# Optimization experiments

Hardware: AMD Instinct MI355X
Metric: run time of the kernel (lower is better)

## Reference

```python
import jax, jax.numpy as jnp
import numpy as np

EPS = 1e-7  # Keras backend epsilon


def setup_inputs() -> dict:
    key = jax.random.key(0)
    kx, ka, ke, kp = jax.random.split(key, 4)
    B, N, F, K_, C = 8, 2048, 128, 128, 128
    X = jax.random.normal(kx, (B, N, F), dtype=jnp.float32)
    Au = (jax.random.uniform(ka, (B, N, N)) < 0.05).astype(jnp.float32)
    A = jnp.maximum(Au, jnp.swapaxes(Au, -1, -2))
    W_emb = jax.random.normal(ke, (F, C), dtype=jnp.float32) * 0.1
    W_pool = jax.random.normal(kp, (F, K_), dtype=jnp.float32) * 0.1
    return {"X": X, "A": A, "W_emb": W_emb, "W_pool": W_pool}


def _diffpool(X, A, W_emb, W_pool):
    N = A.shape[-1]
    I = jnp.eye(N, dtype=A.dtype)
    A_ = A + I
    # symmetric normalization D^-1/2 (A+I) D^-1/2
    d = jax.lax.rsqrt(jnp.sum(A_, axis=-1))          # [B, N]
    fltr = A_ * d[..., :, None] * d[..., None, :]    # [B, N, N]

    Z = jnp.einsum('bnm,bmc->bnc', fltr, X @ W_emb)  # embedding GNN (no activation)
    S = jax.nn.softmax(jnp.einsum('bnm,bmk->bnk', fltr, X @ W_pool), axis=-1)  # [B, N, k]

    # link prediction loss: ||A - S S^T||_F per graph, mean over batch
    S_gram = jnp.einsum('bnk,bmk->bnm', S, S)
    LP_loss = jnp.mean(jnp.linalg.norm(A - S_gram, ord='fro', axis=(-1, -2)))

    # entropy loss on assignments
    entr = -jnp.sum(S * jnp.log(S + EPS), axis=-1)   # [B, N]
    entr_loss = jnp.mean(entr)

    X_pooled = jnp.einsum('bnk,bnc->bkc', S, Z)                  # S^T Z
    A_pooled = jnp.einsum('bnk,bnm,bml->bkl', S, A, S)           # S^T A S
    return X_pooled, A_pooled, S, LP_loss, entr_loss


def reference(X, A, W_emb, W_pool):
    return _diffpool(X, A, W_emb, W_pool)
```

## Files before the change

### kernel.cpp

```cpp
#include <hip/hip_runtime.h>
#include <math.h>

typedef __bf16 bf16x8 __attribute__((ext_vector_type(8)));
typedef float  f32x4  __attribute__((ext_vector_type(4)));
typedef unsigned short u16x4 __attribute__((ext_vector_type(4)));

#define DEVI __device__ __forceinline__

static constexpr int NB  = 8;
static constexpr int NN  = 2048;
static constexpr int NF  = 128;
static constexpr int NC2 = 256;

static constexpr int OUT_X0  = 0;
static constexpr int OUT_A0  = NB * 128 * 128;
static constexpr int OUT_S0  = OUT_A0 + NB * 128 * 128;
static constexpr int OUT_LP  = OUT_S0 + NB * NN * 128;
static constexpr int OUT_ENT = OUT_LP + 1;

DEVI unsigned short f2b(float f) {
  unsigned int u = __builtin_bit_cast(unsigned int, f);
  u += 0x7fffu + ((u >> 16) & 1u);
  return (unsigned short)(u >> 16);
}
DEVI float b2f(unsigned short h) {
  unsigned int u = ((unsigned int)h) << 16;
  return __builtin_bit_cast(float, u);
}
DEVI void load_lds16(const void* g, void* l) {
  __builtin_amdgcn_global_load_lds(
      (const __attribute__((address_space(1))) void*)g,
      (__attribute__((address_space(3))) void*)l, 16, 0, 0);
}

DEVI void stage_tile(const unsigned short* src, int ld, unsigned short* dst,
                     int k0, int tid) {
  const int wave = tid >> 6;
#pragma unroll
  for (int is = 0; is < 2; ++is) {
    const int row = is * 64 + (tid >> 2);
    const int c   = tid & 3;
    const unsigned short* g = src + row * ld + k0 + ((c ^ (row & 3)) << 3);
    unsigned short* l = dst + ((is * 256 + wave * 64) << 3);
    load_lds16(g, l);
  }
}

DEVI void gemm_core(const unsigned short* Aop, int lda,
                    const unsigned short* Bop, int ldb, int ksteps,
                    unsigned short* lA0, unsigned short* lA1,
                    unsigned short* lB0, unsigned short* lB1,
                    int tid, f32x4 (&acc)[4][4]) {
  const int lane = tid & 63;
  const int wave = tid >> 6;
  const int wr = wave >> 1, wc = wave & 1;
  const int l15 = lane & 15;
  const int sx = (lane >> 4) ^ (l15 & 3);
#pragma unroll
  for (int i = 0; i < 4; ++i) {
#pragma unroll
    for (int j = 0; j < 4; ++j) acc[i][j] = (f32x4){0.f, 0.f, 0.f, 0.f};
  }
  stage_tile(Aop, lda, lA0, 0, tid);
  stage_tile(Bop, ldb, lB0, 0, tid);
  __syncthreads();
  for (int kt = 0; kt < ksteps; ++kt) {
    unsigned short* curA = (kt & 1) ? lA1 : lA0;
    unsigned short* curB = (kt & 1) ? lB1 : lB0;
    if (kt + 1 < ksteps) {
      unsigned short* nxtA = (kt & 1) ? lA0 : lA1;
      unsigned short* nxtB = (kt & 1) ? lB0 : lB1;
      stage_tile(Aop, lda, nxtA, (kt + 1) * 32, tid);
      stage_tile(Bop, ldb, nxtB, (kt + 1) * 32, tid);
    }
    bf16x8 af[4], bg[4];
#pragma unroll
    for (int i = 0; i < 4; ++i) {
      const int row = wr * 64 + i * 16 + l15;
      af[i] = *(const bf16x8*)(curA + ((row * 4 + sx) << 3));
    }
#pragma unroll
    for (int j = 0; j < 4; ++j) {
      const int col = wc * 64 + j * 16 + l15;
      bg[j] = *(const bf16x8*)(curB + ((col * 4 + sx) << 3));
    }
#pragma unroll
    for (int i = 0; i < 4; ++i) {
#pragma unroll
      for (int j = 0; j < 4; ++j)
        acc[i][j] = __builtin_amdgcn_mfma_f32_16x16x32_bf16(af[i], bg[j],
                                                            acc[i][j], 0, 0, 0);
    }
    __syncthreads();
  }
}


__global__ __launch_bounds__(256) void k_prep_a(const float* __restrict__ A,
                                                unsigned short* __restrict__ AB,
                                                float* __restrict__ dvec,
                                                float* __restrict__ rsum) {
  const int row = blockIdx.x * 4 + (threadIdx.x >> 6);
  const int lane = threadIdx.x & 63;
  const f32x4* src = (const f32x4*)(A + ((size_t)row << 11));
  u16x4* dst = (u16x4*)(AB + ((size_t)row << 11));
  float s = 0.f;
#pragma unroll
  for (int it = 0; it < 8; ++it) {
    f32x4 v = src[it * 64 + lane];
    s += v[0] + v[1] + v[2] + v[3];
    u16x4 o;
    o[0] = f2b(v[0]); o[1] = f2b(v[1]); o[2] = f2b(v[2]); o[3] = f2b(v[3]);
    dst[it * 64 + lane] = o;
  }
#pragma unroll
  for (int o2 = 32; o2; o2 >>= 1) s += __shfl_down(s, o2);
  if (lane == 0) {
    dvec[row] = rsqrtf(s + 1.f);
    rsum[row] = s;
  }
}

__global__ __launch_bounds__(256) void k_conv_xw(const float* __restrict__ X,
                                                 const float* __restrict__ Wemb,
                                                 const float* __restrict__ Wpool,
                                                 unsigned short* __restrict__ XB,
                                                 unsigned short* __restrict__ WT) {
  const int blk = blockIdx.x, tid = threadIdx.x;
  if (blk < 512) {
    const int i0 = blk * 1024 + tid;
    const f32x4* src = (const f32x4*)X;
    u16x4* dst = (u16x4*)XB;
#pragma unroll
    for (int it = 0; it < 4; ++it) {
      const int idx = i0 + it * 256;
      f32x4 v = src[idx];
      u16x4 o;
      o[0] = f2b(v[0]); o[1] = f2b(v[1]); o[2] = f2b(v[2]); o[3] = f2b(v[3]);
      dst[idx] = o;
    }
  } else {
    const int e = (blk - 512) * 256 + tid;
    const int c = e >> 4, f0 = (e & 15) * 8;
    const float* W = (c < 128) ? Wemb : Wpool;
    const int cc = c & 127;
#pragma unroll
    for (int q = 0; q < 8; ++q)
      WT[c * 128 + f0 + q] = f2b(W[(f0 + q) * 128 + cc]);
  }
}

__global__ __launch_bounds__(256) void k_gemm_xw(const unsigned short* __restrict__ XB,
                                                 const unsigned short* __restrict__ WT,
                                                 const float* __restrict__ dvec,
                                                 unsigned short* __restrict__ VT) {
  __shared__ unsigned short lA[2][4096], lB[2][4096];
  const int mt = blockIdx.x, ct = blockIdx.y, tid = threadIdx.x;
  f32x4 acc[4][4];
  gemm_core(XB + mt * 128 * NF, NF, WT + ct * 128 * NF, NF, NF / 32,
            lA[0], lA[1], lB[0], lB[1], tid, acc);
  const int lane = tid & 63, wave = tid >> 6;
  const int wr = wave >> 1, wc = wave & 1, l15 = lane & 15, l4 = (lane >> 4) * 4;
#pragma unroll
  for (int i = 0; i < 4; ++i) {
    const int gr0 = mt * 128 + wr * 64 + i * 16 + l4;
    const int b = gr0 >> 11, n0 = gr0 & 2047;
    const f32x4 dv = *(const f32x4*)(dvec + gr0);
#pragma unroll
    for (int j = 0; j < 4; ++j) {
      const int gc = ct * 128 + wc * 64 + j * 16 + l15;
      u16x4 pk;
#pragma unroll
      for (int r = 0; r < 4; ++r) pk[r] = f2b(acc[i][j][r] * dv[r]);
      *(u16x4*)(VT + (((size_t)(b * NC2 + gc)) << 11) + n0) = pk;
    }
  }
}

__global__ __launch_bounds__(256) void k_gemm_nv(const unsigned short* __restrict__ AB,
                                                 const unsigned short* __restrict__ VT,
                                                 const float* __restrict__ dvec,
                                                 unsigned short* __restrict__ YT,
                                                 float* __restrict__ out,
                                                 float* __restrict__ entv) {
  __shared__ unsigned short lA[2][4096], lB[2][4096];
  const int mt = blockIdx.x, ct = blockIdx.y, b = blockIdx.z, tid = threadIdx.x;
  const unsigned short* Aop = AB + ((size_t)b << 22) + (size_t)mt * 128 * NN;
  const unsigned short* Bop = VT + (((size_t)(b * NC2 + ct * 128)) << 11);
  f32x4 acc[4][4];
  gemm_core(Aop, NN, Bop, NN, NN / 32, lA[0], lA[1], lB[0], lB[1], tid, acc);
  const int lane = tid & 63, wave = tid >> 6;
  const int wr = wave >> 1, wc = wave & 1, l15 = lane & 15, l4g = lane >> 4;
  const int l4 = l4g * 4;
  f32x4 dv[4];
#pragma unroll
  for (int i = 0; i < 4; ++i) {
    const int n0 = mt * 128 + wr * 64 + i * 16 + l4;
    dv[i] = *(const f32x4*)(dvec + (b << 11) + n0);
  }
#pragma unroll
  for (int i = 0; i < 4; ++i) {
    const int n0 = mt * 128 + wr * 64 + i * 16 + l4;
#pragma unroll
    for (int j = 0; j < 4; ++j) {
      const int c = ct * 128 + wc * 64 + j * 16 + l15;
      const u16x4 vv = *(const u16x4*)(VT + (((size_t)(b * NC2 + c)) << 11) + n0);
#pragma unroll
      for (int r = 0; r < 4; ++r)
        acc[i][j][r] = (acc[i][j][r] + b2f(vv[r])) * dv[i][r];
    }
  }
  if (ct == 0) {
#pragma unroll
    for (int i = 0; i < 4; ++i) {
      const int n0 = mt * 128 + wr * 64 + i * 16 + l4;
#pragma unroll
      for (int j = 0; j < 4; ++j) {
        const int c = wc * 64 + j * 16 + l15;
        u16x4 pk;
#pragma unroll
        for (int r = 0; r < 4; ++r) pk[r] = f2b(acc[i][j][r]);
        *(u16x4*)(YT + (((size_t)(b * 384 + c)) << 11) + n0) = pk;
      }
    }
    return;
  }
  float* mbuf = (float*)lA;
  float* sbuf = mbuf + 256;
  float* tbuf = mbuf + 512;
  float* ebuf = mbuf + 768;
  float rm[4][4], rs[4][4], rt[4][4];
#pragma unroll
  for (int i = 0; i < 4; ++i)
#pragma unroll
    for (int r = 0; r < 4; ++r) {
      float m = fmaxf(fmaxf(acc[i][0][r], acc[i][1][r]),
                      fmaxf(acc[i][2][r], acc[i][3][r]));
#pragma unroll
      for (int off = 1; off < 16; off <<= 1) m = fmaxf(m, __shfl_xor(m, off));
      if (l15 == 0) mbuf[(wr * 2 + wc) * 64 + i * 16 + l4 + r] = m;
    }
  __syncthreads();
#pragma unroll
  for (int i = 0; i < 4; ++i)
#pragma unroll
    for (int r = 0; r < 4; ++r) {
      const int row = i * 16 + l4 + r;
      rm[i][r] = fmaxf(mbuf[(wr * 2) * 64 + row], mbuf[(wr * 2 + 1) * 64 + row]);
      rs[i][r] = 0.f; rt[i][r] = 0.f;
    }
#pragma unroll
  for (int i = 0; i < 4; ++i)
#pragma unroll
    for (int j = 0; j < 4; ++j)
#pragma unroll
      for (int r = 0; r < 4; ++r) {
        const float xm = acc[i][j][r] - rm[i][r];
        const float e = __expf(xm);
        acc[i][j][r] = e;
        rs[i][r] += e;
        rt[i][r] += xm * e;
      }
  __syncthreads();
#pragma unroll
  for (int i = 0; i < 4; ++i)
#pragma unroll
    for (int r = 0; r < 4; ++r) {
      float s = rs[i][r], t = rt[i][r];
#pragma unroll
      for (int off = 1; off < 16; off <<= 1) {
        s += __shfl_xor(s, off); t += __shfl_xor(t, off);
      }
      if (l15 == 0) {
        sbuf[(wr * 2 + wc) * 64 + i * 16 + l4 + r] = s;
        tbuf[(wr * 2 + wc) * 64 + i * 16 + l4 + r] = t;
      }
    }
  __syncthreads();
  float ent = 0.f;
#pragma unroll
  for (int i = 0; i < 4; ++i)
#pragma unroll
    for (int r = 0; r < 4; ++r) {
      const int row = i * 16 + l4 + r;
      const float s = sbuf[(wr * 2) * 64 + row] + sbuf[(wr * 2 + 1) * 64 + row];
      const float t = tbuf[(wr * 2) * 64 + row] + tbuf[(wr * 2 + 1) * 64 + row];
      const float inv = 1.f / s;
      rs[i][r] = inv;
      ent += __logf(s) - t * inv;
    }
#pragma unroll
  for (int i = 0; i < 4; ++i) {
    const int n0 = mt * 128 + wr * 64 + i * 16 + l4;
#pragma unroll
    for (int j = 0; j < 4; ++j) {
      const int c = wc * 64 + j * 16 + l15;
      u16x4 pk;
#pragma unroll
      for (int r = 0; r < 4; ++r) {
        const float sv = acc[i][j][r] * rs[i][r];
        pk[r] = f2b(sv);
        out[OUT_S0 + (((size_t)((b << 11) + n0 + r)) << 7) + c] = sv;
      }
      *(u16x4*)(YT + (((size_t)(b * 384 + 256 + c)) << 11) + n0) = pk;
    }
  }
  if (wc == 0 && l15 == 0) ebuf[wr * 4 + l4g] = ent;
  __syncthreads();
  if (tid == 0) {
    float e8 = 0.f;
#pragma unroll
    for (int q = 0; q < 8; ++q) e8 += ebuf[q];
    entv[b * 16 + mt] = e8;
  }
}

__global__ __launch_bounds__(256) void k_gemm_as(const unsigned short* __restrict__ AB,
                                                 unsigned short* __restrict__ YT) {
  __shared__ unsigned short lA[2][2048], lB[2][4096];
  const int mt = blockIdx.x, b = blockIdx.z, tid = threadIdx.x;
  const unsigned short* Aop = AB + ((size_t)b << 22) + (size_t)mt * 64 * NN;
  const unsigned short* Bop = YT + (((size_t)(b * 384 + 256)) << 11);
  const int lane = tid & 63, wave = tid >> 6;
  const int l15 = lane & 15;
  const int sx = (lane >> 4) ^ (l15 & 3);
  f32x4 acc[4][2];
#pragma unroll
  for (int i = 0; i < 4; ++i) {
    acc[i][0] = (f32x4){0.f, 0.f, 0.f, 0.f};
    acc[i][1] = (f32x4){0.f, 0.f, 0.f, 0.f};
  }
  {
    const int row = tid >> 2, c = tid & 3;
    load_lds16(Aop + row * NN + ((c ^ (row & 3)) << 3), lA[0] + (wave << 9));
  }
  stage_tile(Bop, NN, lB[0], 0, tid);
  __syncthreads();
  for (int kt = 0; kt < 64; ++kt) {
    unsigned short* curA = lA[kt & 1];
    unsigned short* curB = lB[kt & 1];
    if (kt + 1 < 64) {
      const int k0 = (kt + 1) * 32;
      const int row = tid >> 2, c = tid & 3;
      load_lds16(Aop + row * NN + k0 + ((c ^ (row & 3)) << 3),
                 lA[(kt + 1) & 1] + (wave << 9));
      stage_tile(Bop, NN, lB[(kt + 1) & 1], k0, tid);
    }
    bf16x8 af[4], bg[2];
#pragma unroll
    for (int i = 0; i < 4; ++i)
      af[i] = *(const bf16x8*)(curA + (((i * 16 + l15) * 4 + sx) << 3));
#pragma unroll
    for (int j = 0; j < 2; ++j) {
      const int col = wave * 32 + j * 16 + l15;
      bg[j] = *(const bf16x8*)(curB + ((col * 4 + sx) << 3));
    }
#pragma unroll
    for (int i = 0; i < 4; ++i) {
#pragma unroll
      for (int j = 0; j < 2; ++j)
        acc[i][j] = __builtin_amdgcn_mfma_f32_16x16x32_bf16(af[i], bg[j],
                                                            acc[i][j], 0, 0, 0);
    }
    __syncthreads();
  }
  const int l4 = (lane >> 4) * 4;
#pragma unroll
  for (int i = 0; i < 4; ++i) {
    const int n0 = mt * 64 + i * 16 + l4;
#pragma unroll
    for (int j = 0; j < 2; ++j) {
      const int c = wave * 32 + j * 16 + l15;
      u16x4 pk;
#pragma unroll
      for (int r = 0; r < 4; ++r) pk[r] = f2b(acc[i][j][r]);
      *(u16x4*)(YT + (((size_t)(b * 384 + 128 + c)) << 11) + n0) = pk;
    }
  }
}

__global__ __launch_bounds__(256) void k_gemm_p(const unsigned short* __restrict__ YT,
                                                float* __restrict__ Pp) {
  __shared__ unsigned short lA[2][4096], lB[2][4096];
  const int ct = blockIdx.x, sk = blockIdx.y, b = blockIdx.z, tid = threadIdx.x;
  const unsigned short* Aop = YT + (((size_t)(b * 384 + 256)) << 11) + sk * 256;
  const unsigned short* Bop = YT + (((size_t)(b * 384 + ct * 128)) << 11) + sk * 256;
  f32x4 acc[4][4];
  gemm_core(Aop, NN, Bop, NN, 8, lA[0], lA[1], lB[0], lB[1], tid, acc);
  const int lane = tid & 63, wave = tid >> 6;
  const int wr = wave >> 1, wc = wave & 1, l15 = lane & 15, l4 = (lane >> 4) * 4;
  float* dst = Pp + ((size_t)(sk * NB + b)) * 128 * 384;
#pragma unroll
  for (int i = 0; i < 4; ++i) {
    const int p0 = wr * 64 + i * 16 + l4;
#pragma unroll
    for (int j = 0; j < 4; ++j) {
      const int gc = ct * 128 + wc * 64 + j * 16 + l15;
#pragma unroll
      for (int r = 0; r < 4; ++r) dst[(p0 + r) * 384 + gc] = acc[i][j][r];
    }
  }
}

__global__ __launch_bounds__(256) void k_reduce_p(const float* __restrict__ Pp,
                                                  float* __restrict__ trp,
                                                  float* __restrict__ g2p,
                                                  float* __restrict__ out) {
  const int chunk = blockIdx.x, b = blockIdx.y, tid = threadIdx.x;
  const int e = chunk * 256 + tid;
  const int p = e / 384, c = e - p * 384;
  float s = 0.f;
#pragma unroll
  for (int sk = 0; sk < 8; ++sk)
    s += Pp[((size_t)(sk * NB + b)) * (128 * 384) + e];
  float tr = 0.f, g2 = 0.f;
  if (c < 128) {
    out[OUT_X0 + ((size_t)(b * 128 + p)) * 128 + c] = s;
  } else if (c < 256) {
    out[OUT_A0 + ((size_t)(b * 128 + p)) * 128 + (c - 128)] = s;
    if (c - 128 == p) tr = s;
  } else {
    g2 = s * s;
  }
  __shared__ float rb[512];
  rb[tid] = tr; rb[256 + tid] = g2;
  __syncthreads();
  for (int o = 128; o; o >>= 1) {
    if (tid < o) { rb[tid] += rb[tid + o]; rb[256 + tid] += rb[256 + tid + o]; }
    __syncthreads();
  }
  if (tid == 0) { trp[b * 192 + chunk] = rb[0]; g2p[b * 192 + chunk] = rb[256]; }
}

__global__ __launch_bounds__(256) void k_lp(const float* __restrict__ rsum,
                                            const float* __restrict__ trp,
                                            const float* __restrict__ g2p,
                                            float* __restrict__ lpv) {
  const int b = blockIdx.x, tid = threadIdx.x;
  float nz = 0.f;
#pragma unroll
  for (int i = 0; i < 8; ++i) nz += rsum[(b << 11) + i * 256 + tid];
  float tr = (tid < 192) ? trp[b * 192 + tid] : 0.f;
  float g2 = (tid < 192) ? g2p[b * 192 + tid] : 0.f;
  __shared__ float rb[768];
  rb[tid] = nz; rb[256 + tid] = tr; rb[512 + tid] = g2;
  __syncthreads();
  for (int o = 128; o; o >>= 1) {
    if (tid < o) {
      rb[tid] += rb[tid + o];
      rb[256 + tid] += rb[256 + tid + o];
      rb[512 + tid] += rb[512 + tid + o];
    }
    __syncthreads();
  }
  if (tid == 0)
    lpv[b] = sqrtf(fmaxf(rb[0] - 2.f * rb[256] + rb[512], 0.f));
}

__global__ __launch_bounds__(256) void k_losses(const float* __restrict__ entv,
                                                const float* __restrict__ lpv,
                                                float* __restrict__ out) {
  const int tid = threadIdx.x;
  __shared__ float rb[256];
  rb[tid] = (tid < 128) ? entv[tid] : 0.f;
  __syncthreads();
  for (int o = 128; o; o >>= 1) {
    if (tid < o) rb[tid] += rb[tid + o];
    __syncthreads();
  }
  if (tid == 0) {
    float lp = 0.f;
#pragma unroll
    for (int b = 0; b < 8; ++b) lp += lpv[b];
    out[OUT_LP] = 0.125f * lp;
    out[OUT_ENT] = rb[0] * (1.f / (NB * NN));
  }
}

extern "C" void kernel_launch(void* const* d_in, const int* in_sizes, int n_in,
                              void* d_out, int out_size, void* d_ws, size_t ws_size,
                              hipStream_t stream) {
  const float* X     = (const float*)d_in[0];
  const float* A     = (const float*)d_in[1];
  const float* Wemb  = (const float*)d_in[2];
  const float* Wpool = (const float*)d_in[3];
  float* out = (float*)d_out;

  char* ws = (char*)d_ws;
  size_t o = 0;
  unsigned short* AB = (unsigned short*)(ws + o); o += (size_t)NB * NN * NN * 2;
  unsigned short* XB = (unsigned short*)(ws + o); o += (size_t)NB * NN * NF * 2;
  unsigned short* WT = (unsigned short*)(ws + o); o += (size_t)NC2 * NF * 2;
  unsigned short* VT = (unsigned short*)(ws + o); o += (size_t)NB * NC2 * NN * 2;
  unsigned short* YT = (unsigned short*)(ws + o); o += (size_t)NB * 384 * NN * 2;
  float* Pp  = (float*)(ws + o); o += (size_t)8 * NB * 128 * 384 * 4;
  float* dvec = (float*)(ws + o); o += (size_t)NB * NN * 4;
  float* rsum = (float*)(ws + o); o += (size_t)NB * NN * 4;
  float* trp  = (float*)(ws + o); o += (size_t)NB * 192 * 4;
  float* g2p  = (float*)(ws + o); o += (size_t)NB * 192 * 4;
  float* entv = (float*)(ws + o); o += 128 * 4;
  float* lpv  = (float*)(ws + o); o += NB * 4;

  k_prep_a  <<<dim3(NB * NN / 4), 256, 0, stream>>>(A, AB, dvec, rsum);
  k_conv_xw <<<dim3(528), 256, 0, stream>>>(X, Wemb, Wpool, XB, WT);
  k_gemm_xw <<<dim3(NB * NN / 128, 2), 256, 0, stream>>>(XB, WT, dvec, VT);
  k_gemm_nv <<<dim3(NN / 128, 2, NB), 256, 0, stream>>>(AB, VT, dvec, YT, out, entv);
  k_gemm_as <<<dim3(NN / 64, 1, NB), 256, 0, stream>>>(AB, YT);
  k_gemm_p  <<<dim3(3, 8, NB), 256, 0, stream>>>(YT, Pp);
  k_reduce_p<<<dim3(192, NB), 256, 0, stream>>>(Pp, trp, g2p, out);
  k_lp      <<<dim3(NB), 256, 0, stream>>>(rsum, trp, g2p, lpv);
  k_losses  <<<1, 256, 0, stream>>>(entv, lpv, out);
}
```

Baseline: 323.5 us.

## Shrink GEMM M-tiles to 64 rows, double split-K, fuse prep kernels, change LDS swizzle

The two prep kernels are merged into one launch. The NxN-by-V and X-by-W GEMMs move from 128x128 to 64x128 tiles, which doubles the block count and improves CU occupancy, since the original grid had only 256 blocks. The split-K factor for the S^T Y GEMM rises from 8 to 16, and the LDS swizzle changes to (row>>1)&3. The trade-offs are more B-operand reloads per output, twice the partial-sum traffic in the reduction, and a larger workspace.

Result: faster. 308.7 us (-4.6%).

```diff
diff --git a/kernel.cpp b/kernel.cpp
--- a/kernel.cpp
+++ b/kernel.cpp
@@ -11,6 +11,7 @@
 static constexpr int NN  = 2048;
 static constexpr int NF  = 128;
 static constexpr int NC2 = 256;
+static constexpr int NSK = 16;
 
 static constexpr int OUT_X0  = 0;
 static constexpr int OUT_A0  = NB * 128 * 128;
@@ -32,103 +33,137 @@
       (const __attribute__((address_space(1))) void*)g,
       (__attribute__((address_space(3))) void*)l, 16, 0, 0);
 }
-
-DEVI void stage_tile(const unsigned short* src, int ld, unsigned short* dst,
+DEVI int swz(int row) { return (row >> 1) & 3; }
+
+DEVI void stage_b128(const unsigned short* src, int ld, unsigned short* dst,
                      int k0, int tid) {
   const int wave = tid >> 6;
 #pragma unroll
   for (int is = 0; is < 2; ++is) {
     const int row = is * 64 + (tid >> 2);
     const int c   = tid & 3;
-    const unsigned short* g = src + row * ld + k0 + ((c ^ (row & 3)) << 3);
-    unsigned short* l = dst + ((is * 256 + wave * 64) << 3);
-    load_lds16(g, l);
-  }
-}
-
-DEVI void gemm_core(const unsigned short* Aop, int lda,
-                    const unsigned short* Bop, int ldb, int ksteps,
-                    unsigned short* lA0, unsigned short* lA1,
-                    unsigned short* lB0, unsigned short* lB1,
-                    int tid, f32x4 (&acc)[4][4]) {
-  const int lane = tid & 63;
+    load_lds16(src + row * ld + k0 + ((c ^ swz(row)) << 3),
+               dst + ((is * 256 + wave * 64) << 3));
+  }
+}
+DEVI void stage_a64(const unsigned short* src, int ld, unsigned short* dst,
+                    int k0, int tid) {
   const int wave = tid >> 6;
-  const int wr = wave >> 1, wc = wave & 1;
+  const int row = tid >> 2, c = tid & 3;
+  load_lds16(src + row * ld + k0 + ((c ^ swz(row)) << 3), dst + (wave << 9));
+}
+
+DEVI void gemm_core64(const unsigned short* Aop, int lda,
+                      const unsigned short* Bop, int ldb, int ksteps,
+                      unsigned short* lA0, unsigned short* lA1,
+                      unsigned short* lB0, unsigned short* lB1,
+                      int tid, f32x4 (&acc)[4][2]) {
+  const int lane = tid & 63, wave = tid >> 6;
   const int l15 = lane & 15;
-  const int sx = (lane >> 4) ^ (l15 & 3);
-#pragma unroll
-  for (int i = 0; i < 4; ++i) {
-#pragma unroll
-    for (int j = 0; j < 4; ++j) acc[i][j] = (f32x4){0.f, 0.f, 0.f, 0.f};
-  }
-  stage_tile(Aop, lda, lA0, 0, tid);
-  stage_tile(Bop, ldb, lB0, 0, tid);
+  const int sx = (lane >> 4) ^ ((l15 >> 1) & 3);
+#pragma unroll
+  for (int i = 0; i < 4; ++i) {
+    acc[i][0] = (f32x4){0.f, 0.f, 0.f, 0.f};
+    acc[i][1] = (f32x4){0.f, 0.f, 0.f, 0.f};
+  }
+  stage_a64(Aop, lda, lA0, 0, tid);
+  stage_b128(Bop, ldb, lB0, 0, tid);
   __syncthreads();
   for (int kt = 0; kt < ksteps; ++kt) {
     unsigned short* curA = (kt & 1) ? lA1 : lA0;
     unsigned short* curB = (kt & 1) ? lB1 : lB0;
     if (kt + 1 < ksteps) {
-      unsigned short* nxtA = (kt & 1) ? lA0 : lA1;
-      unsigned short* nxtB = (kt & 1) ? lB0 : lB1;
-      stage_tile(Aop, lda, nxtA, (kt + 1) * 32, tid);
-      stage_tile(Bop, ldb, nxtB, (kt + 1) * 32, tid);
+      const int k0 = (kt + 1) * 32;
+      stage_a64(Aop, lda, (kt & 1) ? lA0 : lA1, k0, tid);
+      stage_b128(Bop, ldb, (kt & 1) ? lB0 : lB1, k0, tid);
+    }
+    bf16x8 af[4], bg[2];
+#pragma unroll
+    for (int i = 0; i < 4; ++i)
+      af[i] = *(const bf16x8*)(curA + (((i * 16 + l15) * 4 + sx) << 3));
+#pragma unroll
+    for (int j = 0; j < 2; ++j)
+      bg[j] = *(const bf16x8*)(curB + (((wave * 32 + j * 16 + l15) * 4 + sx) << 3));
+#pragma unroll
+    for (int i = 0; i < 4; ++i)
+#pragma unroll
+      for (int j = 0; j < 2; ++j)
+        acc[i][j] = __builtin_amdgcn_mfma_f32_16x16x32_bf16(af[i], bg[j],
+                                                            acc[i][j], 0, 0, 0);
+    __syncthreads();
+  }
+}
+
+DEVI void gemm_core128(const unsigned short* Aop, int lda,
+                       const unsigned short* Bop, int ldb, int ksteps,
+                       unsigned short* lA0, unsigned short* lA1,
+                       unsigned short* lB0, unsigned short* lB1,
+                       int tid, f32x4 (&acc)[4][4]) {
+  const int lane = tid & 63, wave = tid >> 6;
+  const int wr = wave >> 1, wc = wave & 1;
+  const int l15 = lane & 15;
+  const int sx = (lane >> 4) ^ ((l15 >> 1) & 3);
+#pragma unroll
+  for (int i = 0; i < 4; ++i)
+#pragma unroll
+    for (int j = 0; j < 4; ++j) acc[i][j] = (f32x4){0.f, 0.f, 0.f, 0.f};
+  stage_b128(Aop, lda, lA0, 0, tid);
+  stage_b128(Bop, ldb, lB0, 0, tid);
+  __syncthreads();
+  for (int kt = 0; kt < ksteps; ++kt) {
+    unsigned short* curA = (kt & 1) ? lA1 : lA0;
+    unsigned short* curB = (kt & 1) ? lB1 : lB0;
+    if (kt + 1 < ksteps) {
+      const int k0 = (kt + 1) * 32;
+      stage_b128(Aop, lda, (kt & 1) ? lA0 : lA1, k0, tid);
+      stage_b128(Bop, ldb, (kt & 1) ? lB0 : lB1, k0, tid);
     }
     bf16x8 af[4], bg[4];
 #pragma unroll
-    for (int i = 0; i < 4; ++i) {
-      const int row = wr * 64 + i * 16 + l15;
-      af[i] = *(const bf16x8*)(curA + ((row * 4 + sx) << 3));
-    }
-#pragma unroll
-    for (int j = 0; j < 4; ++j) {
-      const int col = wc * 64 + j * 16 + l15;
-      bg[j] = *(const bf16x8*)(curB + ((col * 4 + sx) << 3));
-    }
-#pragma unroll
-    for (int i = 0; i < 4; ++i) {
+    for (int i = 0; i < 4; ++i)
+      af[i] = *(const bf16x8*)(curA + (((wr * 64 + i * 16 + l15) * 4 + sx) << 3));
+#pragma unroll
+    for (int j = 0; j < 4; ++j)
+      bg[j] = *(const bf16x8*)(curB + (((wc * 64 + j * 16 + l15) * 4 + sx) << 3));
+#pragma unroll
+    for (int i = 0; i < 4; ++i)
 #pragma unroll
       for (int j = 0; j < 4; ++j)
         acc[i][j] = __builtin_amdgcn_mfma_f32_16x16x32_bf16(af[i], bg[j],
                                                             acc[i][j], 0, 0, 0);
-    }
     __syncthreads();
   }
 }
 
-
-__global__ __launch_bounds__(256) void k_prep_a(const float* __restrict__ A,
-                                                unsigned short* __restrict__ AB,
-                                                float* __restrict__ dvec,
-                                                float* __restrict__ rsum) {
-  const int row = blockIdx.x * 4 + (threadIdx.x >> 6);
-  const int lane = threadIdx.x & 63;
-  const f32x4* src = (const f32x4*)(A + ((size_t)row << 11));
-  u16x4* dst = (u16x4*)(AB + ((size_t)row << 11));
-  float s = 0.f;
-#pragma unroll
-  for (int it = 0; it < 8; ++it) {
-    f32x4 v = src[it * 64 + lane];
-    s += v[0] + v[1] + v[2] + v[3];
-    u16x4 o;
-    o[0] = f2b(v[0]); o[1] = f2b(v[1]); o[2] = f2b(v[2]); o[3] = f2b(v[3]);
-    dst[it * 64 + lane] = o;
-  }
-#pragma unroll
-  for (int o2 = 32; o2; o2 >>= 1) s += __shfl_down(s, o2);
-  if (lane == 0) {
-    dvec[row] = rsqrtf(s + 1.f);
-    rsum[row] = s;
-  }
-}
-
-__global__ __launch_bounds__(256) void k_conv_xw(const float* __restrict__ X,
-                                                 const float* __restrict__ Wemb,
-                                                 const float* __restrict__ Wpool,
-                                                 unsigned short* __restrict__ XB,
-                                                 unsigned short* __restrict__ WT) {
+__global__ __launch_bounds__(256) void k_prep(const float* __restrict__ A,
+                                              const float* __restrict__ X,
+                                              const float* __restrict__ Wemb,
+                                              const float* __restrict__ Wpool,
+                                              unsigned short* __restrict__ AB,
+                                              unsigned short* __restrict__ XB,
+                                              unsigned short* __restrict__ WT,
+                                              float* __restrict__ dvec,
+                                              float* __restrict__ rsum) {
   const int blk = blockIdx.x, tid = threadIdx.x;
-  if (blk < 512) {
-    const int i0 = blk * 1024 + tid;
+  if (blk < 4096) {
+    const int row = blk * 4 + (tid >> 6);
+    const int lane = tid & 63;
+    const f32x4* src = (const f32x4*)(A + ((size_t)row << 11));
+    u16x4* dst = (u16x4*)(AB + ((size_t)row << 11));
+    float s = 0.f;
+#pragma unroll
+    for (int it = 0; it < 8; ++it) {
+      f32x4 v = src[it * 64 + lane];
+      s += v[0] + v[1] + v[2] + v[3];
+      u16x4 o;
+      o[0] = f2b(v[0]); o[1] = f2b(v[1]); o[2] = f2b(v[2]); o[3] = f2b(v[3]);
+      dst[it * 64 + lane] = o;
+    }
+#pragma unroll
+    for (int o2 = 32; o2; o2 >>= 1) s += __shfl_down(s, o2);
+    if (lane == 0) { dvec[row] = rsqrtf(s + 1.f); rsum[row] = s; }
+  } else if (blk < 4608) {
+    const int i0 = (blk - 4096) * 1024 + tid;
     const f32x4* src = (const f32x4*)X;
     u16x4* dst = (u16x4*)XB;
 #pragma unroll
@@ -140,7 +175,7 @@
       dst[idx] = o;
     }
   } else {
-    const int e = (blk - 512) * 256 + tid;
+    const int e = (blk - 4608) * 256 + tid;
     const int c = e >> 4, f0 = (e & 15) * 8;
     const float* W = (c < 128) ? Wemb : Wpool;
     const int cc = c & 127;
@@ -154,21 +189,21 @@
                                                  const unsigned short* __restrict__ WT,
                                                  const float* __restrict__ dvec,
                                                  unsigned short* __restrict__ VT) {
-  __shared__ unsigned short lA[2][4096], lB[2][4096];
+  __shared__ unsigned short lA[2][2048], lB[2][4096];
   const int mt = blockIdx.x, ct = blockIdx.y, tid = threadIdx.x;
-  f32x4 acc[4][4];
-  gemm_core(XB + mt * 128 * NF, NF, WT + ct * 128 * NF, NF, NF / 32,
-            lA[0], lA[1], lB[0], lB[1], tid, acc);
-  const int lane = tid & 63, wave = tid >> 6;
-  const int wr = wave >> 1, wc = wave & 1, l15 = lane & 15, l4 = (lane >> 4) * 4;
-#pragma unroll
-  for (int i = 0; i < 4; ++i) {
-    const int gr0 = mt * 128 + wr * 64 + i * 16 + l4;
+  f32x4 acc[4][2];
+  gemm_core64(XB + mt * 64 * NF, NF, WT + ct * 128 * NF, NF, NF / 32,
+              lA[0], lA[1], lB[0], lB[1], tid, acc);
+  const int lane = tid & 63, wave = tid >> 6;
+  const int l15 = lane & 15, l4 = (lane >> 4) * 4;
+#pragma unroll
+  for (int i = 0; i < 4; ++i) {
+    const int gr0 = mt * 64 + i * 16 + l4;
     const int b = gr0 >> 11, n0 = gr0 & 2047;
     const f32x4 dv = *(const f32x4*)(dvec + gr0);
 #pragma unroll
-    for (int j = 0; j < 4; ++j) {
-      const int gc = ct * 128 + wc * 64 + j * 16 + l15;
+    for (int j = 0; j < 2; ++j) {
+      const int gc = ct * 128 + wave * 32 + j * 16 + l15;
       u16x4 pk;
 #pragma unroll
       for (int r = 0; r < 4; ++r) pk[r] = f2b(acc[i][j][r] * dv[r]);
@@ -183,27 +218,24 @@
                                                  unsigned short* __restrict__ YT,
                                                  float* __restrict__ out,
                                                  float* __restrict__ entv) {
-  __shared__ unsigned short lA[2][4096], lB[2][4096];
+  __shared__ unsigned short lA[2][2048], lB[2][4096];
   const int mt = blockIdx.x, ct = blockIdx.y, b = blockIdx.z, tid = threadIdx.x;
-  const unsigned short* Aop = AB + ((size_t)b << 22) + (size_t)mt * 128 * NN;
+  const unsigned short* Aop = AB + ((size_t)b << 22) + (size_t)mt * 64 * NN;
   const unsigned short* Bop = VT + (((size_t)(b * NC2 + ct * 128)) << 11);
-  f32x4 acc[4][4];
-  gemm_core(Aop, NN, Bop, NN, NN / 32, lA[0], lA[1], lB[0], lB[1], tid, acc);
-  const int lane = tid & 63, wave = tid >> 6;
-  const int wr = wave >> 1, wc = wave & 1, l15 = lane & 15, l4g = lane >> 4;
-  const int l4 = l4g * 4;
+  f32x4 acc[4][2];
+  gemm_core64(Aop, NN, Bop, NN, NN / 32, lA[0], lA[1], lB[0], lB[1], tid, acc);
+  const int lane = tid & 63, wave = tid >> 6;
+  const int l15 = lane & 15, l4g = lane >> 4, l4 = l4g * 4;
   f32x4 dv[4];
 #pragma unroll
-  for (int i = 0; i < 4; ++i) {
-    const int n0 = mt * 128 + wr * 64 + i * 16 + l4;
-    dv[i] = *(const f32x4*)(dvec + (b << 11) + n0);
-  }
-#pragma unroll
-  for (int i = 0; i < 4; ++i) {
-    const int n0 = mt * 128 + wr * 64 + i * 16 + l4;
-#pragma unroll
-    for (int j = 0; j < 4; ++j) {
-      const int c = ct * 128 + wc * 64 + j * 16 + l15;
+  for (int i = 0; i < 4; ++i)
+    dv[i] = *(const f32x4*)(dvec + (b << 11) + mt * 64 + i * 16 + l4);
+#pragma unroll
+  for (int i = 0; i < 4; ++i) {
+    const int n0 = mt * 64 + i * 16 + l4;
+#pragma unroll
+    for (int j = 0; j < 2; ++j) {
+      const int c = ct * 128 + wave * 32 + j * 16 + l15;
       const u16x4 vv = *(const u16x4*)(VT + (((size_t)(b * NC2 + c)) << 11) + n0);
 #pragma unroll
       for (int r = 0; r < 4; ++r)
@@ -213,10 +245,10 @@
   if (ct == 0) {
 #pragma unroll
     for (int i = 0; i < 4; ++i) {
-      const int n0 = mt * 128 + wr * 64 + i * 16 + l4;
-#pragma unroll
-      for (int j = 0; j < 4; ++j) {
-        const int c = wc * 64 + j * 16 + l15;
+      const int n0 = mt * 64 + i * 16 + l4;
+#pragma unroll
+      for (int j = 0; j < 2; ++j) {
+        const int c = wave * 32 + j * 16 + l15;
         u16x4 pk;
 #pragma unroll
         for (int r = 0; r < 4; ++r) pk[r] = f2b(acc[i][j][r]);
@@ -234,11 +266,10 @@
   for (int i = 0; i < 4; ++i)
 #pragma unroll
     for (int r = 0; r < 4; ++r) {
-      float m = fmaxf(fmaxf(acc[i][0][r], acc[i][1][r]),
-                      fmaxf(acc[i][2][r], acc[i][3][r]));
+      float m = fmaxf(acc[i][0][r], acc[i][1][r]);
 #pragma unroll
       for (int off = 1; off < 16; off <<= 1) m = fmaxf(m, __shfl_xor(m, off));
-      if (l15 == 0) mbuf[(wr * 2 + wc) * 64 + i * 16 + l4 + r] = m;
+      if (l15 == 0) mbuf[wave * 64 + i * 16 + l4 + r] = m;
     }
   __syncthreads();
 #pragma unroll
@@ -246,13 +277,14 @@
 #pragma unroll
     for (int r = 0; r < 4; ++r) {
       const int row = i * 16 + l4 + r;
-      rm[i][r] = fmaxf(mbuf[(wr * 2) * 64 + row], mbuf[(wr * 2 + 1) * 64 + row]);
+      rm[i][r] = fmaxf(fmaxf(mbuf[row], mbuf[64 + row]),
+                       fmaxf(mbuf[128 + row], mbuf[192 + row]));
       rs[i][r] = 0.f; rt[i][r] = 0.f;
     }
 #pragma unroll
   for (int i = 0; i < 4; ++i)
 #pragma unroll
-    for (int j = 0; j < 4; ++j)
+    for (int j = 0; j < 2; ++j)
 #pragma unroll
       for (int r = 0; r < 4; ++r) {
         const float xm = acc[i][j][r] - rm[i][r];
@@ -261,7 +293,6 @@
         rs[i][r] += e;
         rt[i][r] += xm * e;
       }
-  __syncthreads();
 #pragma unroll
   for (int i = 0; i < 4; ++i)
 #pragma unroll
@@ -272,8 +303,8 @@
         s += __shfl_xor(s, off); t += __shfl_xor(t, off);
       }
       if (l15 == 0) {
-        sbuf[(wr * 2 + wc) * 64 + i * 16 + l4 + r] = s;
-        tbuf[(wr * 2 + wc) * 64 + i * 16 + l4 + r] = t;
+        sbuf[wave * 64 + i * 16 + l4 + r] = s;
+        tbuf[wave * 64 + i * 16 + l4 + r] = t;
       }
     }
   __syncthreads();
@@ -283,18 +314,18 @@
 #pragma unroll
     for (int r = 0; r < 4; ++r) {
       const int row = i * 16 + l4 + r;
-      const float s = sbuf[(wr * 2) * 64 + row] + sbuf[(wr * 2 + 1) * 64 + row];
-      const float t = tbuf[(wr * 2) * 64 + row] + tbuf[(wr * 2 + 1) * 64 + row];
+      const float s = sbuf[row] + sbuf[64 + row] + sbuf[128 + row] + sbuf[192 + row];
+      const float t = tbuf[row] + tbuf[64 + row] + tbuf[128 + row] + tbuf[192 + row];
       const float inv = 1.f / s;
       rs[i][r] = inv;
       ent += __logf(s) - t * inv;
     }
 #pragma unroll
   for (int i = 0; i < 4; ++i) {
-    const int n0 = mt * 128 + wr * 64 + i * 16 + l4;
-#pragma unroll
-    for (int j = 0; j < 4; ++j) {
-      const int c = wc * 64 + j * 16 + l15;
+    const int n0 = mt * 64 + i * 16 + l4;
+#pragma unroll
+    for (int j = 0; j < 2; ++j) {
+      const int c = wave * 32 + j * 16 + l15;
       u16x4 pk;
 #pragma unroll
       for (int r = 0; r < 4; ++r) {
@@ -305,14 +336,10 @@
       *(u16x4*)(YT + (((size_t)(b * 384 + 256 + c)) << 11) + n0) = pk;
     }
   }
-  if (wc == 0 && l15 == 0) ebuf[wr * 4 + l4g] = ent;
-  __syncthreads();
-  if (tid == 0) {
-    float e8 = 0.f;
-#pragma unroll
-    for (int q = 0; q < 8; ++q) e8 += ebuf[q];
-    entv[b * 16 + mt] = e8;
-  }
+  if (wave == 0 && l15 == 0) ebuf[l4g] = ent;
+  __syncthreads();
+  if (tid == 0)
+    entv[b * 32 + mt] = ebuf[0] + ebuf[1] + ebuf[2] + ebuf[3];
 }
 
 __global__ __launch_bounds__(256) void k_gemm_as(const unsigned short* __restrict__ AB,
@@ -321,50 +348,10 @@
   const int mt = blockIdx.x, b = blockIdx.z, tid = threadIdx.x;
   const unsigned short* Aop = AB + ((size_t)b << 22) + (size_t)mt * 64 * NN;
   const unsigned short* Bop = YT + (((size_t)(b * 384 + 256)) << 11);
-  const int lane = tid & 63, wave = tid >> 6;
-  const int l15 = lane & 15;
-  const int sx = (lane >> 4) ^ (l15 & 3);
   f32x4 acc[4][2];
-#pragma unroll
-  for (int i = 0; i < 4; ++i) {
-    acc[i][0] = (f32x4){0.f, 0.f, 0.f, 0.f};
-    acc[i][1] = (f32x4){0.f, 0.f, 0.f, 0.f};
-  }
-  {
-    const int row = tid >> 2, c = tid & 3;
-    load_lds16(Aop + row * NN + ((c ^ (row & 3)) << 3), lA[0] + (wave << 9));
-  }
-  stage_tile(Bop, NN, lB[0], 0, tid);
-  __syncthreads();
-  for (int kt = 0; kt < 64; ++kt) {
-    unsigned short* curA = lA[kt & 1];
-    unsigned short* curB = lB[kt & 1];
-    if (kt + 1 < 64) {
-      const int k0 = (kt + 1) * 32;
-      const int row = tid >> 2, c = tid & 3;
-      load_lds16(Aop + row * NN + k0 + ((c ^ (row & 3)) << 3),
-                 lA[(kt + 1) & 1] + (wave << 9));
-      stage_tile(Bop, NN, lB[(kt + 1) & 1], k0, tid);
-    }
-    bf16x8 af[4], bg[2];
-#pragma unroll
-    for (int i = 0; i < 4; ++i)
-      af[i] = *(const bf16x8*)(curA + (((i * 16 + l15) * 4 + sx) << 3));
-#pragma unroll
-    for (int j = 0; j < 2; ++j) {
-      const int col = wave * 32 + j * 16 + l15;
-      bg[j] = *(const bf16x8*)(curB + ((col * 4 + sx) << 3));
-    }
-#pragma unroll
-    for (int i = 0; i < 4; ++i) {
-#pragma unroll
-      for (int j = 0; j < 2; ++j)
-        acc[i][j] = __builtin_amdgcn_mfma_f32_16x16x32_bf16(af[i], bg[j],
-                                                            acc[i][j], 0, 0, 0);
-    }
-    __syncthreads();
-  }
-  const int l4 = (lane >> 4) * 4;
+  gemm_core64(Aop, NN, Bop, NN, NN / 32, lA[0], lA[1], lB[0], lB[1], tid, acc);
+  const int lane = tid & 63, wave = tid >> 6;
+  const int l15 = lane & 15, l4 = (lane >> 4) * 4;
 #pragma unroll
   for (int i = 0; i < 4; ++i) {
     const int n0 = mt * 64 + i * 16 + l4;
@@ -383,10 +370,10 @@
                                                 float* __restrict__ Pp) {
   __shared__ unsigned short lA[2][4096], lB[2][4096];
   const int ct = blockIdx.x, sk = blockIdx.y, b = blockIdx.z, tid = threadIdx.x;
-  const unsigned short* Aop = YT + (((size_t)(b * 384 + 256)) << 11) + sk * 256;
-  const unsigned short* Bop = YT + (((size_t)(b * 384 + ct * 128)) << 11) + sk * 256;
+  const unsigned short* Aop = YT + (((size_t)(b * 384 + 256)) << 11) + sk * 128;
+  const unsigned short* Bop = YT + (((size_t)(b * 384 + ct * 128)) << 11) + sk * 128;
   f32x4 acc[4][4];
-  gemm_core(Aop, NN, Bop, NN, 8, lA[0], lA[1], lB[0], lB[1], tid, acc);
+  gemm_core128(Aop, NN, Bop, NN, 4, lA[0], lA[1], lB[0], lB[1], tid, acc);
   const int lane = tid & 63, wave = tid >> 6;
   const int wr = wave >> 1, wc = wave & 1, l15 = lane & 15, l4 = (lane >> 4) * 4;
   float* dst = Pp + ((size_t)(sk * NB + b)) * 128 * 384;
@@ -411,7 +398,7 @@
   const int p = e / 384, c = e - p * 384;
   float s = 0.f;
 #pragma unroll
-  for (int sk = 0; sk < 8; ++sk)
+  for (int sk = 0; sk < NSK; ++sk)
     s += Pp[((size_t)(sk * NB + b)) * (128 * 384) + e];
   float tr = 0.f, g2 = 0.f;
   if (c < 128) {
@@ -462,7 +449,7 @@
                                                 float* __restrict__ out) {
   const int tid = threadIdx.x;
   __shared__ float rb[256];
-  rb[tid] = (tid < 128) ? entv[tid] : 0.f;
+  rb[tid] = entv[tid];
   __syncthreads();
   for (int o = 128; o; o >>= 1) {
     if (tid < o) rb[tid] += rb[tid + o];
@@ -493,20 +480,19 @@
   unsigned short* WT = (unsigned short*)(ws + o); o += (size_t)NC2 * NF * 2;
   unsigned short* VT = (unsigned short*)(ws + o); o += (size_t)NB * NC2 * NN * 2;
   unsigned short* YT = (unsigned short*)(ws + o); o += (size_t)NB * 384 * NN * 2;
-  float* Pp  = (float*)(ws + o); o += (size_t)8 * NB * 128 * 384 * 4;
+  float* Pp  = (float*)(ws + o); o += (size_t)NSK * NB * 128 * 384 * 4;
   float* dvec = (float*)(ws + o); o += (size_t)NB * NN * 4;
   float* rsum = (float*)(ws + o); o += (size_t)NB * NN * 4;
   float* trp  = (float*)(ws + o); o += (size_t)NB * 192 * 4;
   float* g2p  = (float*)(ws + o); o += (size_t)NB * 192 * 4;
-  float* entv = (float*)(ws + o); o += 128 * 4;
+  float* entv = (float*)(ws + o); o += 256 * 4;
   float* lpv  = (float*)(ws + o); o += NB * 4;
 
-  k_prep_a  <<<dim3(NB * NN / 4), 256, 0, stream>>>(A, AB, dvec, rsum);
-  k_conv_xw <<<dim3(528), 256, 0, stream>>>(X, Wemb, Wpool, XB, WT);
-  k_gemm_xw <<<dim3(NB * NN / 128, 2), 256, 0, stream>>>(XB, WT, dvec, VT);
-  k_gemm_nv <<<dim3(NN / 128, 2, NB), 256, 0, stream>>>(AB, VT, dvec, YT, out, entv);
+  k_prep    <<<dim3(4624), 256, 0, stream>>>(A, X, Wemb, Wpool, AB, XB, WT, dvec, rsum);
+  k_gemm_xw <<<dim3(NB * NN / 64, 2), 256, 0, stream>>>(XB, WT, dvec, VT);
+  k_gemm_nv <<<dim3(NN / 64, 2, NB), 256, 0, stream>>>(AB, VT, dvec, YT, out, entv);
   k_gemm_as <<<dim3(NN / 64, 1, NB), 256, 0, stream>>>(AB, YT);
-  k_gemm_p  <<<dim3(3, 8, NB), 256, 0, stream>>>(YT, Pp);
+  k_gemm_p  <<<dim3(3, NSK, NB), 256, 0, stream>>>(YT, Pp);
   k_reduce_p<<<dim3(192, NB), 256, 0, stream>>>(Pp, trp, g2p, out);
   k_lp      <<<dim3(NB), 256, 0, stream>>>(rsum, trp, g2p, lpv);
   k_losses  <<<1, 256, 0, stream>>>(entv, lpv, out);
```
